# Performance work log

Hardware: AMD Instinct MI355X
Metric: run time of the kernel (lower is better)

## Reference

```python
import jax, jax.numpy as jnp
import numpy as np

# Layer sizes for each 3-layer LSTM tower (input_dim, hidden_dim), as in the torch module.
SIZES = [(50, 25), (25, 10), (10, 4)]
B = 32768


def _lstm(x, Wih, Whh, b):
    """Single-layer batch-first LSTM (torch gate order i,f,g,o). x: [B,T,Din].
    Returns (ys [B,T,H], h_last [B,H]). b = b_ih + b_hh combined."""
    Bn = x.shape[0]
    H = Whh.shape[1]

    def step(carry, xt):
        h, c = carry
        gates = xt @ Wih.T + h @ Whh.T + b  # [B, 4H]
        i, f, g, o = jnp.split(gates, 4, axis=-1)
        c = jax.nn.sigmoid(f) * c + jax.nn.sigmoid(i) * jnp.tanh(g)
        h = jax.nn.sigmoid(o) * jnp.tanh(c)
        return (h, c), h

    z = jnp.zeros((Bn, H), x.dtype)
    (h_last, _), ys = jax.lax.scan(step, (z, z), jnp.swapaxes(x, 0, 1))
    return jnp.swapaxes(ys, 0, 1), h_last


def _tower(x, params):
    h = None
    for (Wih, Whh, b) in params:
        x, h = _lstm(x, Wih, Whh, b)
    return h  # last layer's final hidden state [B, 4]


def setup_inputs() -> dict:
    key = jax.random.key(0)
    inp = {}
    k_q, k_p, key = jax.random.split(key, 3)
    inp["q"] = jax.random.normal(k_q, (B, 12, 50), jnp.float32)
    inp["p"] = jax.random.normal(k_p, (B, 50, 50), jnp.float32)
    for prefix in ("q", "p"):
        for i, (din, dh) in enumerate(SIZES):
            k1, k2, key = jax.random.split(key, 3)
            inp[f"{prefix}Wih{i}"] = jax.random.normal(k1, (4 * dh, din), jnp.float32) * (1.0 / np.sqrt(din))
            inp[f"{prefix}Whh{i}"] = jax.random.normal(k2, (4 * dh, dh), jnp.float32) * (1.0 / np.sqrt(dh))
            inp[f"{prefix}b{i}"] = jnp.zeros((4 * dh,), jnp.float32)
    k1, key = jax.random.split(key)
    inp["fW"] = jax.random.normal(k1, (2, 4), jnp.float32) * 0.5
    inp["fb"] = jnp.zeros((2,), jnp.float32)
    return inp


def reference(q, p,
              qWih0, qWhh0, qb0, qWih1, qWhh1, qb1, qWih2, qWhh2, qb2,
              pWih0, pWhh0, pb0, pWih1, pWhh1, pb1, pWih2, pWhh2, pb2,
              fW, fb):
    q_params = [(qWih0, qWhh0, qb0), (qWih1, qWhh1, qb1), (qWih2, qWhh2, qb2)]
    p_params = [(pWih0, pWhh0, pb0), (pWih1, pWhh1, pb1), (pWih2, pWhh2, pb2)]
    h_q = _tower(q, q_params)  # [B, 4]
    h_p = _tower(p, p_params)  # [B, 4]
    scores = h_q * h_p
    return jax.nn.softmax(scores @ fW.T + fb, axis=1)  # [B, 2]
```

## Files before the change

kernel.cpp:

```cpp
#include <hip/hip_runtime.h>
#include <cstddef>

#define DEV static __device__ __forceinline__

constexpr int B_TOTAL = 32768;
constexpr int ROWS = 128;
constexpr int NBLK = B_TOTAL / ROWS;

constexpr int WL1_OFF = 7800, WL2_OFF = 9400, W_TOTAL = 9656;
constexpr int H0_STR = 28;
constexpr int H1_STR = 12;
constexpr int HQ_OFF = 0;
constexpr int HP_OFF = B_TOTAL * 4;

DEV float fexp2(float x) { return __builtin_amdgcn_exp2f(x); }
DEV float frcp(float x) { return __builtin_amdgcn_rcpf(x); }
DEV float fsig(float x) { return frcp(1.0f + fexp2(-1.4426950408889634f * x)); }
DEV float ftanh_(float x) { return 2.0f * frcp(1.0f + fexp2(-2.8853900817779268f * x)) - 1.0f; }

DEV float elem4(const float4 v, const int jj) {
  return jj == 0 ? v.x : jj == 1 ? v.y : jj == 2 ? v.z : v.w;
}

template <int NU>
DEV void gfma1(float* __restrict__ g0, float* __restrict__ g1,
               const float4* __restrict__ w, const float va, const float vb) {
#pragma unroll
  for (int u = 0; u < NU; ++u) {
    const float4 wv = w[u];
    g0[4 * u + 0] = fmaf(wv.x, va, g0[4 * u + 0]);
    g0[4 * u + 1] = fmaf(wv.y, va, g0[4 * u + 1]);
    g0[4 * u + 2] = fmaf(wv.z, va, g0[4 * u + 2]);
    g0[4 * u + 3] = fmaf(wv.w, va, g0[4 * u + 3]);
    g1[4 * u + 0] = fmaf(wv.x, vb, g1[4 * u + 0]);
    g1[4 * u + 1] = fmaf(wv.y, vb, g1[4 * u + 1]);
    g1[4 * u + 2] = fmaf(wv.z, vb, g1[4 * u + 2]);
    g1[4 * u + 3] = fmaf(wv.w, vb, g1[4 * u + 3]);
  }
}

template <int NU>
DEV void gfma2(float* __restrict__ a0, float* __restrict__ a1,
               float* __restrict__ b0, float* __restrict__ b1,
               const float4* __restrict__ w,
               const float xat, const float xbt, const float xan, const float xbn) {
#pragma unroll
  for (int u = 0; u < NU; ++u) {
    const float4 wv = w[u];
    a0[4 * u + 0] = fmaf(wv.x, xat, a0[4 * u + 0]);
    a0[4 * u + 1] = fmaf(wv.y, xat, a0[4 * u + 1]);
    a0[4 * u + 2] = fmaf(wv.z, xat, a0[4 * u + 2]);
    a0[4 * u + 3] = fmaf(wv.w, xat, a0[4 * u + 3]);
    a1[4 * u + 0] = fmaf(wv.x, xbt, a1[4 * u + 0]);
    a1[4 * u + 1] = fmaf(wv.y, xbt, a1[4 * u + 1]);
    a1[4 * u + 2] = fmaf(wv.z, xbt, a1[4 * u + 2]);
    a1[4 * u + 3] = fmaf(wv.w, xbt, a1[4 * u + 3]);
    b0[4 * u + 0] = fmaf(wv.x, xan, b0[4 * u + 0]);
    b0[4 * u + 1] = fmaf(wv.y, xan, b0[4 * u + 1]);
    b0[4 * u + 2] = fmaf(wv.z, xan, b0[4 * u + 2]);
    b0[4 * u + 3] = fmaf(wv.w, xan, b0[4 * u + 3]);
    b1[4 * u + 0] = fmaf(wv.x, xbn, b1[4 * u + 0]);
    b1[4 * u + 1] = fmaf(wv.y, xbn, b1[4 * u + 1]);
    b1[4 * u + 2] = fmaf(wv.z, xbn, b1[4 * u + 2]);
    b1[4 * u + 3] = fmaf(wv.w, xbn, b1[4 * u + 3]);
  }
}

template <int NU>
DEV void activ(const float* __restrict__ g, float* __restrict__ c,
               float* __restrict__ hn) {
#pragma unroll
  for (int u = 0; u < NU; ++u) {
    const float gi_ = fsig(g[4 * u + 0]);
    const float gf  = fsig(g[4 * u + 1]);
    const float gg  = ftanh_(g[4 * u + 2]);
    const float go  = fsig(g[4 * u + 3]);
    const float cn  = fmaf(gf, c[u], gi_ * gg);
    c[u] = cn;
    hn[u] = go * ftanh_(cn);
  }
}

template <int NU>
DEV void l0_even(const float* __restrict__ wl,
                 const float* __restrict__ x2a, const float* __restrict__ x2b,
                 const float* h0, const int ra, const int rb, const int u0,
                 float* __restrict__ c, float* __restrict__ hn,
                 float* __restrict__ gb0, float* __restrict__ gb1) {
  float ga0[4 * NU], ga1[4 * NU];
  {
    const float4* bq = reinterpret_cast<const float4*>(wl + 7700) + u0;
#pragma unroll
    for (int u = 0; u < NU; ++u) {
      const float4 b = bq[u];
      ga0[4 * u + 0] = b.x; ga0[4 * u + 1] = b.y; ga0[4 * u + 2] = b.z; ga0[4 * u + 3] = b.w;
      ga1[4 * u + 0] = b.x; ga1[4 * u + 1] = b.y; ga1[4 * u + 2] = b.z; ga1[4 * u + 3] = b.w;
      gb0[4 * u + 0] = b.x; gb0[4 * u + 1] = b.y; gb0[4 * u + 2] = b.z; gb0[4 * u + 3] = b.w;
      gb1[4 * u + 0] = b.x; gb1[4 * u + 1] = b.y; gb1[4 * u + 2] = b.z; gb1[4 * u + 3] = b.w;
    }
  }
#pragma unroll 2
  for (int m = 0; m < 25; ++m) {
    const float2 at = *reinterpret_cast<const float2*>(x2a + 2 * m);
    const float2 an = *reinterpret_cast<const float2*>(x2a + 50 + 2 * m);
    const float2 bt = *reinterpret_cast<const float2*>(x2b + 2 * m);
    const float2 bn = *reinterpret_cast<const float2*>(x2b + 50 + 2 * m);
    const float4* w0 = reinterpret_cast<const float4*>(wl + (2 * m) * 100) + u0;
    const float4* w1 = reinterpret_cast<const float4*>(wl + (2 * m + 1) * 100) + u0;
    gfma2<NU>(ga0, ga1, gb0, gb1, w0, at.x, bt.x, an.x, bn.x);
    gfma2<NU>(ga0, ga1, gb0, gb1, w1, at.y, bt.y, an.y, bn.y);
  }
#pragma unroll 1
  for (int gi = 0; gi < 7; ++gi) {
    const float4 ha = *reinterpret_cast<const float4*>(h0 + ra * H0_STR + 4 * gi);
    const float4 hb = *reinterpret_cast<const float4*>(h0 + rb * H0_STR + 4 * gi);
#pragma unroll
    for (int jj = 0; jj < 4; ++jj) {
      const float4* w = reinterpret_cast<const float4*>(wl + (50 + 4 * gi + jj) * 100) + u0;
      gfma1<NU>(ga0, ga1, w, elem4(ha, jj), elem4(hb, jj));
    }
  }
  activ<NU>(ga0, c, hn);
  activ<NU>(ga1, c + 4, hn + 4);
}

template <int NU>
DEV void l0_odd(const float* __restrict__ wl, const float* h0,
                const int ra, const int rb, const int u0,
                float* __restrict__ c, float* __restrict__ hn,
                float* __restrict__ g0, float* __restrict__ g1) {
#pragma unroll 1
  for (int gi = 0; gi < 7; ++gi) {
    const float4 ha = *reinterpret_cast<const float4*>(h0 + ra * H0_STR + 4 * gi);
    const float4 hb = *reinterpret_cast<const float4*>(h0 + rb * H0_STR + 4 * gi);
#pragma unroll
    for (int jj = 0; jj < 4; ++jj) {
      const float4* w = reinterpret_cast<const float4*>(wl + (50 + 4 * gi + jj) * 100) + u0;
      gfma1<NU>(g0, g1, w, elem4(ha, jj), elem4(hb, jj));
    }
  }
  activ<NU>(g0, c, hn);
  activ<NU>(g1, c + 4, hn + 4);
}

template <int NU>
DEV void l1_fw(const float* __restrict__ wl, const float* h0, const float* h1,
               const int ra, const int rb, const int u0,
               float* __restrict__ c, float* __restrict__ hn) {
  float g0[4 * NU], g1[4 * NU];
  {
    const float4* bq = reinterpret_cast<const float4*>(wl + 1560) + u0;
#pragma unroll
    for (int u = 0; u < NU; ++u) {
      const float4 b = bq[u];
      g0[4 * u + 0] = b.x; g0[4 * u + 1] = b.y; g0[4 * u + 2] = b.z; g0[4 * u + 3] = b.w;
      g1[4 * u + 0] = b.x; g1[4 * u + 1] = b.y; g1[4 * u + 2] = b.z; g1[4 * u + 3] = b.w;
    }
  }
#pragma unroll 1
  for (int gi = 0; gi < 7; ++gi) {
    const float4 ha = *reinterpret_cast<const float4*>(h0 + ra * H0_STR + 4 * gi);
    const float4 hb = *reinterpret_cast<const float4*>(h0 + rb * H0_STR + 4 * gi);
#pragma unroll
    for (int jj = 0; jj < 4; ++jj) {
      const float4* w = reinterpret_cast<const float4*>(wl + (4 * gi + jj) * 40) + u0;
      gfma1<NU>(g0, g1, w, elem4(ha, jj), elem4(hb, jj));
    }
  }
#pragma unroll 1
  for (int gi = 0; gi < 3; ++gi) {
    const float4 ha = *reinterpret_cast<const float4*>(h1 + ra * H1_STR + 4 * gi);
    const float4 hb = *reinterpret_cast<const float4*>(h1 + rb * H1_STR + 4 * gi);
#pragma unroll
    for (int jj = 0; jj < 4; ++jj) {
      const float4* w = reinterpret_cast<const float4*>(wl + (28 + 4 * gi + jj) * 40) + u0;
      gfma1<NU>(g0, g1, w, elem4(ha, jj), elem4(hb, jj));
    }
  }
  activ<NU>(g0, c, hn);
  activ<NU>(g1, c + 2, hn + 2);
}

DEV void l2_fw(const float* __restrict__ wl, const float* h1,
               const int ra, const int rb, float* __restrict__ c,
               float* __restrict__ h2) {
  float g0[16], g1[16];
  {
    const float4* bq = reinterpret_cast<const float4*>(wl + 176);
#pragma unroll
    for (int u = 0; u < 4; ++u) {
      const float4 b = bq[u];
      g0[4 * u + 0] = b.x; g0[4 * u + 1] = b.y; g0[4 * u + 2] = b.z; g0[4 * u + 3] = b.w;
      g1[4 * u + 0] = b.x; g1[4 * u + 1] = b.y; g1[4 * u + 2] = b.z; g1[4 * u + 3] = b.w;
    }
  }
#pragma unroll 1
  for (int gi = 0; gi < 3; ++gi) {
    const float4 ha = *reinterpret_cast<const float4*>(h1 + ra * H1_STR + 4 * gi);
    const float4 hb = *reinterpret_cast<const float4*>(h1 + rb * H1_STR + 4 * gi);
#pragma unroll
    for (int jj = 0; jj < 4; ++jj) {
      const float4* w = reinterpret_cast<const float4*>(wl + (4 * gi + jj) * 16);
      gfma1<4>(g0, g1, w, elem4(ha, jj), elem4(hb, jj));
    }
  }
#pragma unroll
  for (int jj = 0; jj < 4; ++jj) {
    const float4* w = reinterpret_cast<const float4*>(wl + (12 + jj) * 16);
    gfma1<4>(g0, g1, w, h2[jj], h2[4 + jj]);
  }
  activ<4>(g0, c, h2);
  activ<4>(g1, c + 4, h2 + 4);
}

__global__ __launch_bounds__(512, 2) void lstm_towers(
    const float* __restrict__ q, const float* __restrict__ p,
    const float* __restrict__ qWih0, const float* __restrict__ qWhh0, const float* __restrict__ qb0,
    const float* __restrict__ qWih1, const float* __restrict__ qWhh1, const float* __restrict__ qb1,
    const float* __restrict__ qWih2, const float* __restrict__ qWhh2, const float* __restrict__ qb2,
    const float* __restrict__ pWih0, const float* __restrict__ pWhh0, const float* __restrict__ pb0,
    const float* __restrict__ pWih1, const float* __restrict__ pWhh1, const float* __restrict__ pb1,
    const float* __restrict__ pWih2, const float* __restrict__ pWhh2, const float* __restrict__ pb2,
    float* __restrict__ hq_out, float* __restrict__ hp_out) {
  __shared__ float wlds[W_TOTAL];
  __shared__ float h0s[ROWS * H0_STR];
  __shared__ float h1s[2 * ROWS * H1_STR];

  const int tid = threadIdx.x;
  const int r = tid & 63;
  const int wid = tid >> 6;
  const int row0 = blockIdx.x * ROWS;
  const int ra = r, rb = r + 64;

  const int u00 = __builtin_amdgcn_readfirstlane(
      wid < 2 ? 4 * wid : (wid < 7 ? 8 + 3 * (wid - 2) : 23));
  const int u01 = __builtin_amdgcn_readfirstlane(
      wid < 6 ? 2 * (wid - 2) : 8 + (wid - 6));

  const float* wl0 = wlds;
  const float* wl1 = wlds + WL1_OFF;
  const float* wl2 = wlds + WL2_OFF;

#pragma unroll 1
  for (int phase = 0; phase < 2; ++phase) {
    const bool isp = (phase == 1);
    const float* __restrict__ x = isp ? p : q;
    const int T = isp ? 50 : 12;
    const float* Wih0 = isp ? pWih0 : qWih0; const float* Whh0 = isp ? pWhh0 : qWhh0;
    const float* b0g  = isp ? pb0   : qb0;
    const float* Wih1 = isp ? pWih1 : qWih1; const float* Whh1 = isp ? pWhh1 : qWhh1;
    const float* b1g  = isp ? pb1   : qb1;
    const float* Wih2 = isp ? pWih2 : qWih2; const float* Whh2 = isp ? pWhh2 : qWhh2;
    const float* b2g  = isp ? pb2   : qb2;
    float* __restrict__ hout_g = isp ? hp_out : hq_out;

    __syncthreads();

    for (int e = tid; e < W_TOTAL; e += 512) {
      float v = 0.0f;
      if (e < WL1_OFF) {
        const int j = e / 100, k = e % 100, u = k >> 2, gt = k & 3, rr = gt * 25 + u;
        if (j < 50) v = Wih0[rr * 50 + j];
        else if (j < 75) v = Whh0[rr * 25 + (j - 50)];
        else if (j == 77) v = b0g[gt * 25 + u];
      } else if (e < WL2_OFF) {
        const int i = e - WL1_OFF, j = i / 40, k = i % 40, u = k >> 2, gt = k & 3;
        const int rr = gt * 10 + u;
        if (j < 25) v = Wih1[rr * 25 + j];
        else if (j >= 28 && j < 38) v = Whh1[rr * 10 + (j - 28)];
        else if (j == 39) v = b1g[gt * 10 + u];
      } else {
        const int i = e - WL2_OFF, j = i / 16, k = i % 16, u = k >> 2, gt = k & 3;
        const int rr = gt * 4 + u;
        if (j < 10) v = Wih2[rr * 10 + j];
        else if (j == 11) v = b2g[gt * 4 + u];
        else if (j >= 12) v = Whh2[rr * 4 + (j - 12)];
      }
      wlds[e] = v;
    }
    for (int i = tid; i < ROWS * H0_STR; i += 512) h0s[i] = 0.0f;
    for (int i = tid; i < 2 * ROWS * H1_STR; i += 512) h1s[i] = 0.0f;

    float c0[8] = {}, hn0[8];
    float c1[4] = {}, hn1[4];
    float c2[8] = {}, h2r[8] = {};
    float gb0[16], gb1[16];

    const float* x2a = x + (size_t)(row0 + ra) * T * 50;
    const float* x2b = x + (size_t)(row0 + rb) * T * 50;

    __syncthreads();

    int s = 0;
#pragma unroll 1
    for (int tp = 0; tp < T; tp += 2) {
      if (wid < 2)      l0_even<4>(wl0, x2a, x2b, h0s, ra, rb, u00, c0, hn0, gb0, gb1);
      else if (wid < 7) l0_even<3>(wl0, x2a, x2b, h0s, ra, rb, u00, c0, hn0, gb0, gb1);
      else              l0_even<2>(wl0, x2a, x2b, h0s, ra, rb, u00, c0, hn0, gb0, gb1);
      __syncthreads();
      {
        float* da = &h0s[ra * H0_STR + u00];
        float* db = &h0s[rb * H0_STR + u00];
        if (wid < 2) {
          da[0] = hn0[0]; da[1] = hn0[1]; da[2] = hn0[2]; da[3] = hn0[3];
          db[0] = hn0[4]; db[1] = hn0[5]; db[2] = hn0[6]; db[3] = hn0[7];
        } else if (wid < 7) {
          da[0] = hn0[0]; da[1] = hn0[1]; da[2] = hn0[2];
          db[0] = hn0[4]; db[1] = hn0[5]; db[2] = hn0[6];
        } else {
          da[0] = hn0[0]; da[1] = hn0[1];
          db[0] = hn0[4]; db[1] = hn0[5];
        }
      }
      __syncthreads();
      {
        const float* h1rd = h1s + s * (ROWS * H1_STR);
        float* h1wr = h1s + (s ^ 1) * (ROWS * H1_STR);
        if (wid >= 2 && wid < 6) l1_fw<2>(wl1, h0s, h1rd, ra, rb, u01, c1, hn1);
        else if (wid >= 6)       l1_fw<1>(wl1, h0s, h1rd, ra, rb, u01, c1, hn1);
        if (wid >= 2) {
          float* ea = &h1wr[ra * H1_STR + u01];
          float* eb = &h1wr[rb * H1_STR + u01];
          if (wid < 6) { ea[0] = hn1[0]; ea[1] = hn1[1]; eb[0] = hn1[2]; eb[1] = hn1[3]; }
          else         { ea[0] = hn1[0]; eb[0] = hn1[2]; }
        }
        __syncthreads();
        if (wid == 7) l2_fw(wl2, h1wr, ra, rb, c2, h2r);
      }
      s ^= 1;
      if (wid < 2)      l0_odd<4>(wl0, h0s, ra, rb, u00, c0, hn0, gb0, gb1);
      else if (wid < 7) l0_odd<3>(wl0, h0s, ra, rb, u00, c0, hn0, gb0, gb1);
      else              l0_odd<2>(wl0, h0s, ra, rb, u00, c0, hn0, gb0, gb1);
      __syncthreads();
      {
        float* da = &h0s[ra * H0_STR + u00];
        float* db = &h0s[rb * H0_STR + u00];
        if (wid < 2) {
          da[0] = hn0[0]; da[1] = hn0[1]; da[2] = hn0[2]; da[3] = hn0[3];
          db[0] = hn0[4]; db[1] = hn0[5]; db[2] = hn0[6]; db[3] = hn0[7];
        } else if (wid < 7) {
          da[0] = hn0[0]; da[1] = hn0[1]; da[2] = hn0[2];
          db[0] = hn0[4]; db[1] = hn0[5]; db[2] = hn0[6];
        } else {
          da[0] = hn0[0]; da[1] = hn0[1];
          db[0] = hn0[4]; db[1] = hn0[5];
        }
      }
      __syncthreads();
      {
        const float* h1rd = h1s + s * (ROWS * H1_STR);
        float* h1wr = h1s + (s ^ 1) * (ROWS * H1_STR);
        if (wid >= 2 && wid < 6) l1_fw<2>(wl1, h0s, h1rd, ra, rb, u01, c1, hn1);
        else if (wid >= 6)       l1_fw<1>(wl1, h0s, h1rd, ra, rb, u01, c1, hn1);
        if (wid >= 2) {
          float* ea = &h1wr[ra * H1_STR + u01];
          float* eb = &h1wr[rb * H1_STR + u01];
          if (wid < 6) { ea[0] = hn1[0]; ea[1] = hn1[1]; eb[0] = hn1[2]; eb[1] = hn1[3]; }
          else         { ea[0] = hn1[0]; eb[0] = hn1[2]; }
        }
        __syncthreads();
        if (wid == 7) l2_fw(wl2, h1wr, ra, rb, c2, h2r);
      }
      s ^= 1;
      x2a += 100; x2b += 100;
    }
    if (wid == 7) {
      reinterpret_cast<float4*>(hout_g)[row0 + ra] =
          make_float4(h2r[0], h2r[1], h2r[2], h2r[3]);
      reinterpret_cast<float4*>(hout_g)[row0 + rb] =
          make_float4(h2r[4], h2r[5], h2r[6], h2r[7]);
    }
  }
}

__global__ __launch_bounds__(256) void combine_head(
    const float* __restrict__ hq, const float* __restrict__ hp,
    const float* __restrict__ fW, const float* __restrict__ fb,
    float* __restrict__ out) {
  const int b = blockIdx.x * blockDim.x + (int)threadIdx.x;
  if (b >= B_TOTAL) return;
  const float4 vq = reinterpret_cast<const float4*>(hq)[b];
  const float4 vp = reinterpret_cast<const float4*>(hp)[b];
  const float s0 = vq.x * vp.x, s1 = vq.y * vp.y, s2 = vq.z * vp.z, s3 = vq.w * vp.w;
  float l0 = fb[0], l1 = fb[1];
  l0 = fmaf(s0, fW[0], l0); l0 = fmaf(s1, fW[1], l0); l0 = fmaf(s2, fW[2], l0); l0 = fmaf(s3, fW[3], l0);
  l1 = fmaf(s0, fW[4], l1); l1 = fmaf(s1, fW[5], l1); l1 = fmaf(s2, fW[6], l1); l1 = fmaf(s3, fW[7], l1);
  const float m = fmaxf(l0, l1);
  const float e0 = fexp2(1.4426950408889634f * (l0 - m));
  const float e1 = fexp2(1.4426950408889634f * (l1 - m));
  const float inv = frcp(e0 + e1);
  reinterpret_cast<float2*>(out)[b] = make_float2(e0 * inv, e1 * inv);
}

extern "C" void kernel_launch(void* const* d_in, const int* in_sizes, int n_in,
                              void* d_out, int out_size, void* d_ws, size_t ws_size,
                              hipStream_t stream) {
  (void)in_sizes; (void)n_in; (void)out_size; (void)ws_size;
  const float* q = (const float*)d_in[0];
  const float* p = (const float*)d_in[1];
  float* ws = (float*)d_ws;

  lstm_towers<<<NBLK, 512, 0, stream>>>(
      q, p,
      (const float*)d_in[2], (const float*)d_in[3], (const float*)d_in[4],
      (const float*)d_in[5], (const float*)d_in[6], (const float*)d_in[7],
      (const float*)d_in[8], (const float*)d_in[9], (const float*)d_in[10],
      (const float*)d_in[11], (const float*)d_in[12], (const float*)d_in[13],
      (const float*)d_in[14], (const float*)d_in[15], (const float*)d_in[16],
      (const float*)d_in[17], (const float*)d_in[18], (const float*)d_in[19],
      ws + HQ_OFF, ws + HP_OFF);

  combine_head<<<B_TOTAL / 256, 256, 0, stream>>>(
      ws + HQ_OFF, ws + HP_OFF,
      (const float*)d_in[20], (const float*)d_in[21], (float*)d_out);
}
```

Measured before the change: 1.589 ms.

## Double block to 1024 threads and spread hidden units over 16 waves

Blocks grow from 8 to 16 wavefronts. The layer-0 hidden units are redistributed so each wave owns 1–2 units instead of 2–4, layer 1 runs on waves 6–15 with one unit each, and layer 2 moves to wave 0. Inner h-recurrence loops are fully unrolled and the input loop unroll is raised. The aim is shorter per-wave serial dot-product chains and more waves to hide LDS latency, at the cost of more barrier participants, more redundant x loads per row, and losing the two-blocks-per-CU launch bound.

```diff
diff --git a/kernel.cpp b/kernel.cpp
--- a/kernel.cpp
+++ b/kernel.cpp
@@ -99,7 +99,7 @@
       gb1[4 * u + 0] = b.x; gb1[4 * u + 1] = b.y; gb1[4 * u + 2] = b.z; gb1[4 * u + 3] = b.w;
     }
   }
-#pragma unroll 2
+#pragma unroll 5
   for (int m = 0; m < 25; ++m) {
     const float2 at = *reinterpret_cast<const float2*>(x2a + 2 * m);
     const float2 an = *reinterpret_cast<const float2*>(x2a + 50 + 2 * m);
@@ -110,7 +110,7 @@
     gfma2<NU>(ga0, ga1, gb0, gb1, w0, at.x, bt.x, an.x, bn.x);
     gfma2<NU>(ga0, ga1, gb0, gb1, w1, at.y, bt.y, an.y, bn.y);
   }
-#pragma unroll 1
+#pragma unroll
   for (int gi = 0; gi < 7; ++gi) {
     const float4 ha = *reinterpret_cast<const float4*>(h0 + ra * H0_STR + 4 * gi);
     const float4 hb = *reinterpret_cast<const float4*>(h0 + rb * H0_STR + 4 * gi);
@@ -129,7 +129,7 @@
                 const int ra, const int rb, const int u0,
                 float* __restrict__ c, float* __restrict__ hn,
                 float* __restrict__ g0, float* __restrict__ g1) {
-#pragma unroll 1
+#pragma unroll
   for (int gi = 0; gi < 7; ++gi) {
     const float4 ha = *reinterpret_cast<const float4*>(h0 + ra * H0_STR + 4 * gi);
     const float4 hb = *reinterpret_cast<const float4*>(h0 + rb * H0_STR + 4 * gi);
@@ -157,7 +157,7 @@
       g1[4 * u + 0] = b.x; g1[4 * u + 1] = b.y; g1[4 * u + 2] = b.z; g1[4 * u + 3] = b.w;
     }
   }
-#pragma unroll 1
+#pragma unroll
   for (int gi = 0; gi < 7; ++gi) {
     const float4 ha = *reinterpret_cast<const float4*>(h0 + ra * H0_STR + 4 * gi);
     const float4 hb = *reinterpret_cast<const float4*>(h0 + rb * H0_STR + 4 * gi);
@@ -167,7 +167,7 @@
       gfma1<NU>(g0, g1, w, elem4(ha, jj), elem4(hb, jj));
     }
   }
-#pragma unroll 1
+#pragma unroll
   for (int gi = 0; gi < 3; ++gi) {
     const float4 ha = *reinterpret_cast<const float4*>(h1 + ra * H1_STR + 4 * gi);
     const float4 hb = *reinterpret_cast<const float4*>(h1 + rb * H1_STR + 4 * gi);
@@ -194,7 +194,7 @@
       g1[4 * u + 0] = b.x; g1[4 * u + 1] = b.y; g1[4 * u + 2] = b.z; g1[4 * u + 3] = b.w;
     }
   }
-#pragma unroll 1
+#pragma unroll
   for (int gi = 0; gi < 3; ++gi) {
     const float4 ha = *reinterpret_cast<const float4*>(h1 + ra * H1_STR + 4 * gi);
     const float4 hb = *reinterpret_cast<const float4*>(h1 + rb * H1_STR + 4 * gi);
@@ -213,7 +213,7 @@
   activ<4>(g1, c + 4, h2 + 4);
 }
 
-__global__ __launch_bounds__(512, 2) void lstm_towers(
+__global__ __launch_bounds__(1024) void lstm_towers(
     const float* __restrict__ q, const float* __restrict__ p,
     const float* __restrict__ qWih0, const float* __restrict__ qWhh0, const float* __restrict__ qb0,
     const float* __restrict__ qWih1, const float* __restrict__ qWhh1, const float* __restrict__ qb1,
@@ -232,10 +232,8 @@
   const int row0 = blockIdx.x * ROWS;
   const int ra = r, rb = r + 64;
 
-  const int u00 = __builtin_amdgcn_readfirstlane(
-      wid < 2 ? 4 * wid : (wid < 7 ? 8 + 3 * (wid - 2) : 23));
-  const int u01 = __builtin_amdgcn_readfirstlane(
-      wid < 6 ? 2 * (wid - 2) : 8 + (wid - 6));
+  const int u00 = __builtin_amdgcn_readfirstlane(wid < 9 ? 2 * wid : wid + 9);
+  const int u01 = __builtin_amdgcn_readfirstlane(wid >= 6 ? wid - 6 : 0);
 
   const float* wl0 = wlds;
   const float* wl1 = wlds + WL1_OFF;
@@ -256,7 +254,7 @@
 
     __syncthreads();
 
-    for (int e = tid; e < W_TOTAL; e += 512) {
+    for (int e = tid; e < W_TOTAL; e += 1024) {
       float v = 0.0f;
       if (e < WL1_OFF) {
         const int j = e / 100, k = e % 100, u = k >> 2, gt = k & 3, rr = gt * 25 + u;
@@ -278,13 +276,13 @@
       }
       wlds[e] = v;
     }
-    for (int i = tid; i < ROWS * H0_STR; i += 512) h0s[i] = 0.0f;
-    for (int i = tid; i < 2 * ROWS * H1_STR; i += 512) h1s[i] = 0.0f;
+    for (int i = tid; i < ROWS * H0_STR; i += 1024) h0s[i] = 0.0f;
+    for (int i = tid; i < 2 * ROWS * H1_STR; i += 1024) h1s[i] = 0.0f;
 
     float c0[8] = {}, hn0[8];
     float c1[4] = {}, hn1[4];
     float c2[8] = {}, h2r[8] = {};
-    float gb0[16], gb1[16];
+    float gb0[8], gb1[8];
 
     const float* x2a = x + (size_t)(row0 + ra) * T * 50;
     const float* x2b = x + (size_t)(row0 + rb) * T * 50;
@@ -294,77 +292,63 @@
     int s = 0;
 #pragma unroll 1
     for (int tp = 0; tp < T; tp += 2) {
-      if (wid < 2)      l0_even<4>(wl0, x2a, x2b, h0s, ra, rb, u00, c0, hn0, gb0, gb1);
-      else if (wid < 7) l0_even<3>(wl0, x2a, x2b, h0s, ra, rb, u00, c0, hn0, gb0, gb1);
-      else              l0_even<2>(wl0, x2a, x2b, h0s, ra, rb, u00, c0, hn0, gb0, gb1);
+      if (wid < 9) l0_even<2>(wl0, x2a, x2b, h0s, ra, rb, u00, c0, hn0, gb0, gb1);
+      else         l0_even<1>(wl0, x2a, x2b, h0s, ra, rb, u00, c0, hn0, gb0, gb1);
       __syncthreads();
       {
         float* da = &h0s[ra * H0_STR + u00];
         float* db = &h0s[rb * H0_STR + u00];
-        if (wid < 2) {
-          da[0] = hn0[0]; da[1] = hn0[1]; da[2] = hn0[2]; da[3] = hn0[3];
-          db[0] = hn0[4]; db[1] = hn0[5]; db[2] = hn0[6]; db[3] = hn0[7];
-        } else if (wid < 7) {
-          da[0] = hn0[0]; da[1] = hn0[1]; da[2] = hn0[2];
-          db[0] = hn0[4]; db[1] = hn0[5]; db[2] = hn0[6];
-        } else {
+        if (wid < 9) {
           da[0] = hn0[0]; da[1] = hn0[1];
           db[0] = hn0[4]; db[1] = hn0[5];
+        } else {
+          da[0] = hn0[0];
+          db[0] = hn0[4];
         }
       }
       __syncthreads();
       {
         const float* h1rd = h1s + s * (ROWS * H1_STR);
         float* h1wr = h1s + (s ^ 1) * (ROWS * H1_STR);
-        if (wid >= 2 && wid < 6) l1_fw<2>(wl1, h0s, h1rd, ra, rb, u01, c1, hn1);
-        else if (wid >= 6)       l1_fw<1>(wl1, h0s, h1rd, ra, rb, u01, c1, hn1);
-        if (wid >= 2) {
-          float* ea = &h1wr[ra * H1_STR + u01];
-          float* eb = &h1wr[rb * H1_STR + u01];
-          if (wid < 6) { ea[0] = hn1[0]; ea[1] = hn1[1]; eb[0] = hn1[2]; eb[1] = hn1[3]; }
-          else         { ea[0] = hn1[0]; eb[0] = hn1[2]; }
+        if (wid >= 6) {
+          l1_fw<1>(wl1, h0s, h1rd, ra, rb, u01, c1, hn1);
+          h1wr[ra * H1_STR + u01] = hn1[0];
+          h1wr[rb * H1_STR + u01] = hn1[2];
         }
         __syncthreads();
-        if (wid == 7) l2_fw(wl2, h1wr, ra, rb, c2, h2r);
+        if (wid == 0) l2_fw(wl2, h1wr, ra, rb, c2, h2r);
       }
       s ^= 1;
-      if (wid < 2)      l0_odd<4>(wl0, h0s, ra, rb, u00, c0, hn0, gb0, gb1);
-      else if (wid < 7) l0_odd<3>(wl0, h0s, ra, rb, u00, c0, hn0, gb0, gb1);
-      else              l0_odd<2>(wl0, h0s, ra, rb, u00, c0, hn0, gb0, gb1);
+      if (wid < 9) l0_odd<2>(wl0, h0s, ra, rb, u00, c0, hn0, gb0, gb1);
+      else         l0_odd<1>(wl0, h0s, ra, rb, u00, c0, hn0, gb0, gb1);
       __syncthreads();
       {
         float* da = &h0s[ra * H0_STR + u00];
         float* db = &h0s[rb * H0_STR + u00];
-        if (wid < 2) {
-          da[0] = hn0[0]; da[1] = hn0[1]; da[2] = hn0[2]; da[3] = hn0[3];
-          db[0] = hn0[4]; db[1] = hn0[5]; db[2] = hn0[6]; db[3] = hn0[7];
-        } else if (wid < 7) {
-          da[0] = hn0[0]; da[1] = hn0[1]; da[2] = hn0[2];
-          db[0] = hn0[4]; db[1] = hn0[5]; db[2] = hn0[6];
-        } else {
+        if (wid < 9) {
           da[0] = hn0[0]; da[1] = hn0[1];
           db[0] = hn0[4]; db[1] = hn0[5];
+        } else {
+          da[0] = hn0[0];
+          db[0] = hn0[4];
         }
       }
       __syncthreads();
       {
         const float* h1rd = h1s + s * (ROWS * H1_STR);
         float* h1wr = h1s + (s ^ 1) * (ROWS * H1_STR);
-        if (wid >= 2 && wid < 6) l1_fw<2>(wl1, h0s, h1rd, ra, rb, u01, c1, hn1);
-        else if (wid >= 6)       l1_fw<1>(wl1, h0s, h1rd, ra, rb, u01, c1, hn1);
-        if (wid >= 2) {
-          float* ea = &h1wr[ra * H1_STR + u01];
-          float* eb = &h1wr[rb * H1_STR + u01];
-          if (wid < 6) { ea[0] = hn1[0]; ea[1] = hn1[1]; eb[0] = hn1[2]; eb[1] = hn1[3]; }
-          else         { ea[0] = hn1[0]; eb[0] = hn1[2]; }
+        if (wid >= 6) {
+          l1_fw<1>(wl1, h0s, h1rd, ra, rb, u01, c1, hn1);
+          h1wr[ra * H1_STR + u01] = hn1[0];
+          h1wr[rb * H1_STR + u01] = hn1[2];
         }
         __syncthreads();
-        if (wid == 7) l2_fw(wl2, h1wr, ra, rb, c2, h2r);
+        if (wid == 0) l2_fw(wl2, h1wr, ra, rb, c2, h2r);
       }
       s ^= 1;
       x2a += 100; x2b += 100;
     }
-    if (wid == 7) {
+    if (wid == 0) {
       reinterpret_cast<float4*>(hout_g)[row0 + ra] =
           make_float4(h2r[0], h2r[1], h2r[2], h2r[3]);
       reinterpret_cast<float4*>(hout_g)[row0 + rb] =
@@ -400,7 +384,7 @@
   const float* p = (const float*)d_in[1];
   float* ws = (float*)d_ws;
 
-  lstm_towers<<<NBLK, 512, 0, stream>>>(
+  lstm_towers<<<NBLK, 1024, 0, stream>>>(
       q, p,
       (const float*)d_in[2], (const float*)d_in[3], (const float*)d_in[4],
       (const float*)d_in[5], (const float*)d_in[6], (const float*)d_in[7],
```

Result: slower. 2.068 ms (+30.2%).
